# Performance work log

Hardware: AMD Instinct MI355X
Metric: run time of the kernel (lower is better)

The kernel has to match this reference:

```python
import jax, jax.numpy as jnp
import numpy as np

TEMPERATURE = 0.07
EPS = 1e-8
B, D, C = 4096, 512, 10


def setup_inputs() -> dict:
    key = jax.random.key(0)
    k1, k2 = jax.random.split(key)
    features = jax.random.normal(k1, (B, D), dtype=jnp.float32)
    cls = jax.random.randint(k2, (B,), 0, C)
    labels = jax.nn.one_hot(cls, C, dtype=jnp.float32)  # [B, C] one-hot
    return {"features": features, "labels": labels}


def reference(features, labels):
    b = features.shape[0]
    # L2-normalize rows
    feats = features / jnp.linalg.norm(features, axis=1, keepdims=True)
    sim = jnp.clip(feats @ feats.T / TEMPERATURE, -20.0, 20.0)  # [B, B]
    eye = jnp.eye(b, dtype=bool)
    sim = jnp.where(eye, -jnp.inf, sim)  # mask self-similarity

    labels_norm = labels / (labels.sum(axis=1, keepdims=True) + EPS)
    label_sim = labels_norm @ labels_norm.T  # [B, B]
    label_sim = jnp.where(eye, 0.0, label_sim)
    pos_mask = label_sim > 0.1  # [B, B] bool

    exp_sim = jnp.exp(sim)  # diag -> exp(-inf) = 0
    pos_sum = jnp.sum(jnp.where(pos_mask, exp_sim, 0.0), axis=1)  # [B]
    all_sum = jnp.sum(exp_sim, axis=1)  # diag already zero => off-diagonal sum
    loss_i = -jnp.log(pos_sum / (all_sum + EPS) + EPS)  # [B]

    valid = jnp.any(pos_mask, axis=1)  # rows with >=1 positive
    n_valid = jnp.sum(valid.astype(jnp.float32))
    total = jnp.sum(jnp.where(valid, loss_i, 0.0))
    return jnp.where(n_valid > 0, total / n_valid, 0.0)
```

## Files before the change

### kernel.cpp

```cpp
#include <hip/hip_runtime.h>


#define B_ROWS 4096
#define D_DIM  512
#define C_CLS  10
#define NT     64
#define NTILES (NT * (NT + 1) / 2)

typedef __bf16 bf16x8 __attribute__((ext_vector_type(8)));
typedef float  f32x4  __attribute__((ext_vector_type(4)));

__device__ __forceinline__ void load_lds16(const __bf16* g, __bf16* l) {
  __builtin_amdgcn_global_load_lds(
      (const __attribute__((address_space(1))) unsigned int*)g,
      (__attribute__((address_space(3))) unsigned int*)l, 16, 0, 0);
}

__global__ __launch_bounds__(256) void prep_kernel(
    const float* __restrict__ feats, const float* __restrict__ labels,
    __bf16* __restrict__ F, int* __restrict__ cls,
    float* __restrict__ pos_sum, float* __restrict__ all_sum) {
  const int w = threadIdx.x >> 6, lane = threadIdx.x & 63;
  const int row = blockIdx.x * 4 + w;
  const float* fr = feats + (size_t)row * D_DIM;
  float4 v0 = ((const float4*)fr)[2 * lane];
  float4 v1 = ((const float4*)fr)[2 * lane + 1];
  float ss = v0.x*v0.x + v0.y*v0.y + v0.z*v0.z + v0.w*v0.w
           + v1.x*v1.x + v1.y*v1.y + v1.z*v1.z + v1.w*v1.w;
  #pragma unroll
  for (int m = 1; m < 64; m <<= 1) ss += __shfl_xor(ss, m, 64);
  float inv = 1.0f / sqrtf(ss);

  bf16x8 o;
  o[0] = (__bf16)(v0.x * inv); o[1] = (__bf16)(v0.y * inv);
  o[2] = (__bf16)(v0.z * inv); o[3] = (__bf16)(v0.w * inv);
  o[4] = (__bf16)(v1.x * inv); o[5] = (__bf16)(v1.y * inv);
  o[6] = (__bf16)(v1.z * inv); o[7] = (__bf16)(v1.w * inv);
  *(bf16x8*)(F + (size_t)row * D_DIM + 8 * lane) = o;

  float lv = (lane < C_CLS) ? labels[(size_t)row * C_CLS + lane] : 0.f;
  unsigned long long m = __ballot(lv > 0.5f);
  if (lane == 0) {
    cls[row] = (int)(__ffsll((long long)m) - 1);
    pos_sum[row] = 0.f;
    all_sum[row] = 0.f;
  }
}

__global__ __launch_bounds__(256) void sim_kernel(
    const __bf16* __restrict__ F, const int* __restrict__ cls,
    float* __restrict__ pos_sum, float* __restrict__ all_sum) {
  __shared__ __align__(16) __bf16 Abuf[64 * 64];
  __shared__ __align__(16) __bf16 Bbuf[64 * 64];
  __shared__ int clsA[64], clsB[64];

  int rem = blockIdx.x, bi = 0, rowlen = NT;
  while (rem >= rowlen) { rem -= rowlen; ++bi; --rowlen; }
  const int bj = bi + rem;
  const int i0 = bi * 64, j0 = bj * 64;
  const bool offdiag = (bi != bj);

  const int t = threadIdx.x;
  const int w = t >> 6;
  const int lane = t & 63;
  const int q = lane >> 4;
  const int cl = lane & 15;

  if (t < 64)       clsA[t]      = cls[i0 + t];
  else if (t < 128) clsB[t - 64] = cls[j0 + t - 64];

  f32x4 acc[4];
  #pragma unroll
  for (int c = 0; c < 4; ++c) acc[c] = (f32x4){0.f, 0.f, 0.f, 0.f};

  const int srow = lane >> 3;
  const int sg   = (lane & 7) ^ srow;

  for (int k0 = 0; k0 < D_DIM; k0 += 64) {
    __syncthreads();
    #pragma unroll
    for (int r = 0; r < 2; ++r) {
      const int rowbase = w * 16 + r * 8;
      load_lds16(F + (size_t)(i0 + rowbase + srow) * D_DIM + k0 + sg * 8,
                 &Abuf[rowbase * 64]);
      load_lds16(F + (size_t)(j0 + rowbase + srow) * D_DIM + k0 + sg * 8,
                 &Bbuf[rowbase * 64]);
    }
    __syncthreads();

    #pragma unroll
    for (int kk = 0; kk < 64; kk += 32) {
      const int g = (kk >> 3) + q;
      const int cc = g ^ (cl & 7);
      bf16x8 af = *(const bf16x8*)&Abuf[(16 * w + cl) * 64 + cc * 8];
      #pragma unroll
      for (int c = 0; c < 4; ++c) {
        bf16x8 bfr = *(const bf16x8*)&Bbuf[(16 * c + cl) * 64 + cc * 8];
        acc[c] = __builtin_amdgcn_mfma_f32_16x16x32_bf16(af, bfr, acc[c], 0, 0, 0);
      }
    }
  }

  const float invT = 1.0f / 0.07f;
  float sum_all[4] = {0.f, 0.f, 0.f, 0.f};
  float sum_pos[4] = {0.f, 0.f, 0.f, 0.f};
  float cs_all[4]  = {0.f, 0.f, 0.f, 0.f};
  float cs_pos[4]  = {0.f, 0.f, 0.f, 0.f};

  #pragma unroll
  for (int c = 0; c < 4; ++c) {
    const int jloc = 16*c + cl;
    const int gj = j0 + jloc;
    const int cj = clsB[jloc];
    #pragma unroll
    for (int r = 0; r < 4; ++r) {
      const int iloc = 16*w + q*4 + r;
      const int gi = i0 + iloc;
      float s = acc[c][r] * invT;
      s = fminf(fmaxf(s, -20.f), 20.f);
      const bool diag = (gi == gj);
      float e = diag ? 0.f : __expf(s);
      sum_all[r] += e;
      cs_all[c] += e;
      if (!diag && cj == clsA[iloc]) { sum_pos[r] += e; cs_pos[c] += e; }
    }
  }

  #pragma unroll
  for (int r = 0; r < 4; ++r) {
    float sa = sum_all[r], sp = sum_pos[r];
    #pragma unroll
    for (int m = 1; m < 16; m <<= 1) {
      sa += __shfl_xor(sa, m, 64);
      sp += __shfl_xor(sp, m, 64);
    }
    if (cl == 0) {
      const int gi = i0 + 16*w + q*4 + r;
      atomicAdd(&all_sum[gi], sa);
      atomicAdd(&pos_sum[gi], sp);
    }
  }

  if (offdiag) {
    #pragma unroll
    for (int c = 0; c < 4; ++c) {
      float sa = cs_all[c], sp = cs_pos[c];
      sa += __shfl_xor(sa, 16, 64); sa += __shfl_xor(sa, 32, 64);
      sp += __shfl_xor(sp, 16, 64); sp += __shfl_xor(sp, 32, 64);
      if (q == 0) {
        const int gj = j0 + 16*c + cl;
        atomicAdd(&all_sum[gj], sa);
        atomicAdd(&pos_sum[gj], sp);
      }
    }
  }
}

__global__ __launch_bounds__(256) void finalize_kernel(
    const float* __restrict__ pos_sum, const float* __restrict__ all_sum,
    float* __restrict__ out) {
  __shared__ float redT[4], redC[4];
  const int t = threadIdx.x;
  float total = 0.f, cnt = 0.f;
  for (int i = t; i < B_ROWS; i += 256) {
    float ps = pos_sum[i], as = all_sum[i];
    if (ps > 0.f) {
      total += -logf(ps / (as + 1e-8f) + 1e-8f);
      cnt += 1.f;
    }
  }
  #pragma unroll
  for (int m = 1; m < 64; m <<= 1) {
    total += __shfl_xor(total, m, 64);
    cnt   += __shfl_xor(cnt, m, 64);
  }
  if ((t & 63) == 0) { redT[t >> 6] = total; redC[t >> 6] = cnt; }
  __syncthreads();
  if (t == 0) {
    float T = 0.f, Cn = 0.f;
    #pragma unroll
    for (int i = 0; i < 4; ++i) { T += redT[i]; Cn += redC[i]; }
    out[0] = (Cn > 0.f) ? (T / Cn) : 0.f;
  }
}

extern "C" void kernel_launch(void* const* d_in, const int* in_sizes, int n_in,
                              void* d_out, int out_size, void* d_ws, size_t ws_size,
                              hipStream_t stream) {
  const float* features = (const float*)d_in[0];
  const float* labels   = (const float*)d_in[1];
  float* out = (float*)d_out;

  __bf16* F       = (__bf16*)d_ws;
  int*    cls     = (int*)((char*)d_ws + (size_t)B_ROWS * D_DIM * 2);
  float*  pos_sum = (float*)((char*)cls + B_ROWS * sizeof(int));
  float*  all_sum = pos_sum + B_ROWS;

  prep_kernel<<<B_ROWS / 4, 256, 0, stream>>>(features, labels, F, cls,
                                              pos_sum, all_sum);
  sim_kernel<<<NTILES, 256, 0, stream>>>(F, cls, pos_sum, all_sum);
  finalize_kernel<<<1, 256, 0, stream>>>(pos_sum, all_sum, out);
}
```

Measured before the change: 98.00 us.

## Replace global row-sum atomics with per-tile partial buffers and parallel finalize

The similarity kernel no longer issues global float atomics for row and column sums. Each tile now writes its 64 row partials and 64 column partials into a dense per-tile-pair buffer, with column partials combined through LDS atomics first. Finalize becomes a 64-block reduction over these partials, followed by atomic accumulation of totals and a tiny divide kernel. This removes global atomic contention in the hot kernel, at the cost of more global memory traffic and an extra kernel launch.

Result: faster. 93.70 us (-4.4%).

```diff
diff --git a/kernel.cpp b/kernel.cpp
--- a/kernel.cpp
+++ b/kernel.cpp
@@ -19,7 +19,7 @@
 __global__ __launch_bounds__(256) void prep_kernel(
     const float* __restrict__ feats, const float* __restrict__ labels,
     __bf16* __restrict__ F, int* __restrict__ cls,
-    float* __restrict__ pos_sum, float* __restrict__ all_sum) {
+    float* __restrict__ totals) {
   const int w = threadIdx.x >> 6, lane = threadIdx.x & 63;
   const int row = blockIdx.x * 4 + w;
   const float* fr = feats + (size_t)row * D_DIM;
@@ -40,19 +40,18 @@
 
   float lv = (lane < C_CLS) ? labels[(size_t)row * C_CLS + lane] : 0.f;
   unsigned long long m = __ballot(lv > 0.5f);
-  if (lane == 0) {
-    cls[row] = (int)(__ffsll((long long)m) - 1);
-    pos_sum[row] = 0.f;
-    all_sum[row] = 0.f;
-  }
+  if (lane == 0) cls[row] = (int)(__ffsll((long long)m) - 1);
+  if (blockIdx.x == 0 && threadIdx.x == 0) { totals[0] = 0.f; totals[1] = 0.f; }
 }
 
 __global__ __launch_bounds__(256) void sim_kernel(
     const __bf16* __restrict__ F, const int* __restrict__ cls,
-    float* __restrict__ pos_sum, float* __restrict__ all_sum) {
+    float* __restrict__ P_all, float* __restrict__ P_pos) {
   __shared__ __align__(16) __bf16 Abuf[64 * 64];
   __shared__ __align__(16) __bf16 Bbuf[64 * 64];
   __shared__ int clsA[64], clsB[64];
+  __shared__ float g_row_all[64], g_row_pos[64];
+  __shared__ float g_col_all[64], g_col_pos[64];
 
   int rem = blockIdx.x, bi = 0, rowlen = NT;
   while (rem >= rowlen) { rem -= rowlen; ++bi; --rowlen; }
@@ -68,6 +67,7 @@
 
   if (t < 64)       clsA[t]      = cls[i0 + t];
   else if (t < 128) clsB[t - 64] = cls[j0 + t - 64];
+  if (t < 64) { g_col_all[t] = 0.f; g_col_pos[t] = 0.f; }
 
   f32x4 acc[4];
   #pragma unroll
@@ -135,9 +135,9 @@
       sp += __shfl_xor(sp, m, 64);
     }
     if (cl == 0) {
-      const int gi = i0 + 16*w + q*4 + r;
-      atomicAdd(&all_sum[gi], sa);
-      atomicAdd(&pos_sum[gi], sp);
+      const int rloc = 16*w + q*4 + r;
+      g_row_all[rloc] = sa;
+      g_row_pos[rloc] = sp;
     }
   }
 
@@ -148,40 +148,62 @@
       sa += __shfl_xor(sa, 16, 64); sa += __shfl_xor(sa, 32, 64);
       sp += __shfl_xor(sp, 16, 64); sp += __shfl_xor(sp, 32, 64);
       if (q == 0) {
-        const int gj = j0 + 16*c + cl;
-        atomicAdd(&all_sum[gj], sa);
-        atomicAdd(&pos_sum[gj], sp);
+        atomicAdd(&g_col_all[16*c + cl], sa);
+        atomicAdd(&g_col_pos[16*c + cl], sp);
       }
     }
   }
+  __syncthreads();
+
+  const size_t base_row = ((size_t)bi * 64 + bj) * 64;
+  if (w == 0) {
+    P_all[base_row + lane] = g_row_all[lane];
+    P_pos[base_row + lane] = g_row_pos[lane];
+  } else if (w == 1 && offdiag) {
+    const size_t base_col = ((size_t)bj * 64 + bi) * 64;
+    P_all[base_col + lane] = g_col_all[lane];
+    P_pos[base_col + lane] = g_col_pos[lane];
+  }
 }
 
 __global__ __launch_bounds__(256) void finalize_kernel(
-    const float* __restrict__ pos_sum, const float* __restrict__ all_sum,
-    float* __restrict__ out) {
-  __shared__ float redT[4], redC[4];
+    const float* __restrict__ P_all, const float* __restrict__ P_pos,
+    float* __restrict__ totals) {
+  __shared__ float Sall[4096], Spos[4096];
+  const int s = blockIdx.x;
   const int t = threadIdx.x;
-  float total = 0.f, cnt = 0.f;
-  for (int i = t; i < B_ROWS; i += 256) {
-    float ps = pos_sum[i], as = all_sum[i];
-    if (ps > 0.f) {
-      total += -logf(ps / (as + 1e-8f) + 1e-8f);
-      cnt += 1.f;
-    }
-  }
-  #pragma unroll
-  for (int m = 1; m < 64; m <<= 1) {
-    total += __shfl_xor(total, m, 64);
-    cnt   += __shfl_xor(cnt, m, 64);
-  }
-  if ((t & 63) == 0) { redT[t >> 6] = total; redC[t >> 6] = cnt; }
+  for (int i = t; i < 4096; i += 256) {
+    Sall[i] = P_all[(size_t)s * 4096 + i];
+    Spos[i] = P_pos[(size_t)s * 4096 + i];
+  }
   __syncthreads();
-  if (t == 0) {
-    float T = 0.f, Cn = 0.f;
-    #pragma unroll
-    for (int i = 0; i < 4; ++i) { T += redT[i]; Cn += redC[i]; }
-    out[0] = (Cn > 0.f) ? (T / Cn) : 0.f;
-  }
+  if (t < 64) {
+    float a = 0.f, p = 0.f;
+    #pragma unroll 8
+    for (int k = 0; k < 64; ++k) {
+      a += Sall[k * 64 + t];
+      p += Spos[k * 64 + t];
+    }
+    float loss = 0.f, cnt = 0.f;
+    if (p > 0.f) {
+      loss = -logf(p / (a + 1e-8f) + 1e-8f);
+      cnt = 1.f;
+    }
+    #pragma unroll
+    for (int m = 1; m < 64; m <<= 1) {
+      loss += __shfl_xor(loss, m, 64);
+      cnt  += __shfl_xor(cnt, m, 64);
+    }
+    if (t == 0) {
+      atomicAdd(&totals[0], loss);
+      atomicAdd(&totals[1], cnt);
+    }
+  }
+}
+
+__global__ void div_kernel(const float* __restrict__ totals,
+                           float* __restrict__ out) {
+  out[0] = (totals[1] > 0.f) ? (totals[0] / totals[1]) : 0.f;
 }
 
 extern "C" void kernel_launch(void* const* d_in, const int* in_sizes, int n_in,
@@ -191,13 +213,14 @@
   const float* labels   = (const float*)d_in[1];
   float* out = (float*)d_out;
 
-  __bf16* F       = (__bf16*)d_ws;
-  int*    cls     = (int*)((char*)d_ws + (size_t)B_ROWS * D_DIM * 2);
-  float*  pos_sum = (float*)((char*)cls + B_ROWS * sizeof(int));
-  float*  all_sum = pos_sum + B_ROWS;
-
-  prep_kernel<<<B_ROWS / 4, 256, 0, stream>>>(features, labels, F, cls,
-                                              pos_sum, all_sum);
-  sim_kernel<<<NTILES, 256, 0, stream>>>(F, cls, pos_sum, all_sum);
-  finalize_kernel<<<1, 256, 0, stream>>>(pos_sum, all_sum, out);
-}
+  __bf16* F      = (__bf16*)d_ws;
+  int*    cls    = (int*)((char*)d_ws + (size_t)B_ROWS * D_DIM * 2);
+  float*  P_all  = (float*)((char*)cls + B_ROWS * sizeof(int));
+  float*  P_pos  = P_all + (size_t)NT * NT * 64;
+  float*  totals = P_pos + (size_t)NT * NT * 64;
+
+  prep_kernel<<<B_ROWS / 4, 256, 0, stream>>>(features, labels, F, cls, totals);
+  sim_kernel<<<NTILES, 256, 0, stream>>>(F, cls, P_all, P_pos);
+  finalize_kernel<<<NT, 256, 0, stream>>>(P_all, P_pos, totals);
+  div_kernel<<<1, 1, 0, stream>>>(totals, out);
+}
```
